# Performance work log

Hardware: AMD Instinct MI355X
Metric: run time of the kernel (lower is better)

Reference implementation:

```python
import jax, jax.numpy as jnp
import numpy as np
from jax import lax

D_MODEL = 1024
D_FF = 4096
NUM_EXPERTS = 24
TOP_K = 2
B, S = 2, 2048


def setup_inputs() -> dict:
    key = jax.random.key(0)
    ks = jax.random.split(key, 5)
    x = jax.random.normal(ks[0], (B, S, D_MODEL), dtype=jnp.float32)
    gate_w = jax.random.normal(ks[1], (D_MODEL, NUM_EXPERTS), dtype=jnp.float32) * 0.02
    gate_b = jnp.zeros((NUM_EXPERTS,), dtype=jnp.float32)
    w1 = jax.random.normal(ks[2], (NUM_EXPERTS, D_MODEL, D_FF), dtype=jnp.float32) * 0.02
    b1 = jnp.zeros((NUM_EXPERTS, D_FF), dtype=jnp.float32)
    w2 = jax.random.normal(ks[3], (NUM_EXPERTS, D_FF, D_MODEL), dtype=jnp.float32) * 0.02
    b2 = jnp.zeros((NUM_EXPERTS, D_MODEL), dtype=jnp.float32)
    return {"x": x, "gate_w": gate_w, "gate_b": gate_b,
            "w1": w1, "b1": b1, "w2": w2, "b2": b2}


def reference(x, gate_w, gate_b, w1, b1, w2, b2):
    b, s, d = x.shape
    t = b * s
    xf = x.reshape(t, d)  # [T, d]
    scores = xf @ gate_w + gate_b  # [T, E]
    top_val, top_idx = lax.top_k(scores, TOP_K)  # [T, k]
    prob = jax.nn.softmax(top_val, axis=-1)  # softmax over the top-k logits
    # scatter top-k probabilities into dense per-expert combine weights [T, E]
    combine = jnp.zeros((t, NUM_EXPERTS), dtype=x.dtype)
    combine = combine.at[jnp.arange(t)[:, None], top_idx].add(prob)

    def body(acc, expert):
        w1e, b1e, w2e, b2e, ce = expert  # ce: [T]
        h = jax.nn.gelu(xf @ w1e + b1e, approximate=False)  # exact GELU as torch default
        y = h @ w2e + b2e  # [T, d]
        return acc + ce[:, None] * y, None

    out, _ = lax.scan(body, jnp.zeros_like(xf), (w1, b1, w2, b2, combine.T))
    return out.reshape(b, s, d)
```

## Files before the change

### kernel.cpp

```cpp
#include <hip/hip_runtime.h>
#include <math.h>

#define DM 1024
#define DF 4096
#define NE 24
#define T_TOK 4096
#define T2 (T_TOK*2)

#define BM 128
#define BN 128
#define BK 64
#define MTILES 8
#define NK1 (DM / BK)
#define NK2 (DF / BK)

typedef __attribute__((ext_vector_type(4))) float f32x4;
typedef __attribute__((ext_vector_type(2))) float f32x2;
typedef __attribute__((ext_vector_type(8))) short s16x8;

static __device__ __forceinline__ unsigned short f2bf(float f) {
    unsigned int u = __float_as_uint(f);
    unsigned int r = u + 0x7fffu + ((u >> 16) & 1u);
    return (unsigned short)(r >> 16);
}

static __device__ __forceinline__ unsigned int cvtpk(float lo, float hi) {
    unsigned int r;
    asm("v_cvt_pk_bf16_f32 %0, %1, %2" : "=v"(r) : "v"(lo), "v"(hi));
    return r;
}

#define GLL(gsrc, ldst)                                                          \
    __builtin_amdgcn_global_load_lds(                                            \
        (const __attribute__((address_space(1))) void*)(gsrc),                   \
        (__attribute__((address_space(3))) void*)(ldst), 16, 0, 0)


__global__ void k_transpose_gw(const float* __restrict__ gw, float* __restrict__ gwT) {
    int e = blockIdx.x;
    for (int d = threadIdx.x; d < DM; d += blockDim.x)
        gwT[e * DM + d] = gw[d * NE + e];
}

__global__ void k_gate(const float* __restrict__ x, const float* __restrict__ gwT,
                       const float* __restrict__ gb,
                       int* __restrict__ idx, float* __restrict__ prob) {
    int wave = threadIdx.x >> 6;
    int lane = threadIdx.x & 63;
    int t = blockIdx.x * 4 + wave;
    if (t >= T_TOK) return;
    const float* xr = x + (size_t)t * DM;
    float acc[NE];
#pragma unroll
    for (int e = 0; e < NE; e++) acc[e] = 0.f;
    for (int i = 0; i < DM / 64; i++) {
        int d = lane + i * 64;
        float xv = xr[d];
#pragma unroll
        for (int e = 0; e < NE; e++) acc[e] = fmaf(xv, gwT[e * DM + d], acc[e]);
    }
#pragma unroll
    for (int e = 0; e < NE; e++) {
        float v = acc[e];
        for (int off = 32; off >= 1; off >>= 1) v += __shfl_xor(v, off);
        acc[e] = v;
    }
    if (lane == 0) {
        float v1 = -1e30f, v2 = -1e30f;
        int i1 = -1, i2 = -1;
        for (int e = 0; e < NE; e++) {
            float s = acc[e] + gb[e];
            if (s > v1) { v2 = v1; i2 = i1; v1 = s; i1 = e; }
            else if (s > v2) { v2 = s; i2 = e; }
        }
        float e2 = expf(v2 - v1);
        float inv = 1.f / (1.f + e2);
        idx[t * 2] = i1; idx[t * 2 + 1] = i2;
        prob[t * 2] = inv; prob[t * 2 + 1] = e2 * inv;
    }
}


__global__ __launch_bounds__(1024)
void k_route(const int* __restrict__ idx, int* __restrict__ counts,
             int* __restrict__ offsets, int* __restrict__ slot_tok,
             int* __restrict__ pair_slot) {
    __shared__ int cnt[NE], offs[NE], cur[NE];
    const int tid = threadIdx.x;
    if (tid < NE) cnt[tid] = 0;
    __syncthreads();
    for (int i = tid; i < T2; i += 1024) atomicAdd(&cnt[idx[i]], 1);
    __syncthreads();
    if (tid == 0) {
        int s = 0;
        for (int e = 0; e < NE; e++) {
            offs[e] = s; offsets[e] = s; counts[e] = cnt[e]; s += cnt[e];
        }
    }
    if (tid < NE) cur[tid] = 0;
    __syncthreads();
    for (int i = tid; i < T2; i += 1024) {
        int e = idx[i];
        int pos = offs[e] + atomicAdd(&cur[e], 1);
        slot_tok[pos] = i >> 1;
        pair_slot[i] = pos;
    }
}

__global__ void k_gather(const float* __restrict__ x, const int* __restrict__ slot_tok,
                         unsigned short* __restrict__ Xg) {
    int s = blockIdx.x;
    int tok = slot_tok[s];
    const float4* src = (const float4*)(x + (size_t)tok * DM);
    ushort4* dst = (ushort4*)(Xg + (size_t)s * DM);
    for (int i = threadIdx.x; i < DM / 4; i += blockDim.x) {
        float4 v = src[i];
        ushort4 o;
        o.x = f2bf(v.x); o.y = f2bf(v.y); o.z = f2bf(v.z); o.w = f2bf(v.w);
        dst[i] = o;
    }
}

__global__ void k_combine(const float* __restrict__ Y, const int* __restrict__ pair_slot,
                          const float* __restrict__ prob, const int* __restrict__ idx,
                          const float* __restrict__ b2, float* __restrict__ out) {
    int t = blockIdx.x;
    int s1 = pair_slot[t * 2], s2 = pair_slot[t * 2 + 1];
    int e1 = idx[t * 2], e2 = idx[t * 2 + 1];
    float p1 = prob[t * 2], p2 = prob[t * 2 + 1];
    const float4* y1 = (const float4*)(Y + (size_t)s1 * DM);
    const float4* y2 = (const float4*)(Y + (size_t)s2 * DM);
    const float4* ba = (const float4*)(b2 + (size_t)e1 * DM);
    const float4* bb = (const float4*)(b2 + (size_t)e2 * DM);
    float4* o = (float4*)(out + (size_t)t * DM);
    int i = threadIdx.x;
    float4 a = y1[i], b = y2[i], c = ba[i], d = bb[i];
    float4 r;
    r.x = p1 * (a.x + c.x) + p2 * (b.x + d.x);
    r.y = p1 * (a.y + c.y) + p2 * (b.y + d.y);
    r.z = p1 * (a.z + c.z) + p2 * (b.z + d.z);
    r.w = p1 * (a.w + c.w) + p2 * (b.w + d.w);
    o[i] = r;
}


__global__ __launch_bounds__(512)
void k_mm1(const unsigned short* __restrict__ Xg, const float* __restrict__ w1,
           const float* __restrict__ b1, const int* __restrict__ counts,
           const int* __restrict__ offsets, unsigned short* __restrict__ H) {
    const int TOT = NE * MTILES * (DF / BN);
    int work = (blockIdx.x & 7) * (TOT >> 3) + (blockIdx.x >> 3);
    const int mt = work % MTILES;
    const int en = work / MTILES;
    const int e  = en >> 5;
    const int n0 = (en & 31) * BN;
    const int ne = counts[e];
    const int m0 = mt * BM;
    if (m0 >= ne) return;
    const int rows = min(BM, ne - m0);
    const int slotbase = offsets[e] + m0;

    __shared__ unsigned short As[2][BM * BK];
    __shared__ unsigned short Bs[BN * BK];

    const int tid  = threadIdx.x;
    const int lane = tid & 63;
    const int w    = tid >> 6;
    const int wm   = w >> 1, wn = w & 1;

    const float* w1e = w1 + (size_t)e * DM * DF;
    const int arow = lane >> 3;
    const int gchunk = ((lane & 7) ^ arow) * 8;

    const int swz0 = ((lane >> 4) ^ (lane & 7)) << 4;
    const int swz1 = ((4 | (lane >> 4)) ^ (lane & 7)) << 4;
    const char* Arow0 = (const char*)As[0] + (wm * 32 + (lane & 15)) * 128;
    const char* Arow1 = (const char*)As[1] + (wm * 32 + (lane & 15)) * 128;
    const char* Brow  = (const char*)Bs + (wn * 64 + (lane & 15)) * 128;

    const int np = (tid & 63) * 2;
    const int ckw = w;
    char* BsW0 = (char*)Bs + (np + 0) * 128 + ((ckw ^ ((np + 0) & 7)) << 4);
    char* BsW1 = (char*)Bs + (np + 1) * 128 + ((ckw ^ ((np + 1) & 7)) << 4);

    f32x4 acc[2][4];
#pragma unroll
    for (int a = 0; a < 2; a++)
#pragma unroll
        for (int b = 0; b < 4; b++) acc[a][b] = (f32x4)0.f;

    f32x2 L[8];
    auto loadB = [&](int k0) {
#pragma unroll
        for (int j = 0; j < 8; j++)
            L[j] = *(const f32x2*)(w1e + (size_t)(k0 + w * 8 + j) * DF + n0 + np);
    };
    auto stageA = [&](int buf, int k0) {
#pragma unroll
        for (int q = 0; q < 2; q++) {
            int row = (w * 2 + q) * 8 + arow;
            GLL(Xg + (size_t)(slotbase + row) * DM + k0 + gchunk,
                &As[buf][(w * 2 + q) * 512]);
        }
    };

    stageA(0, 0);
    loadB(0);
#pragma unroll 1
    for (int kt = 0; kt < NK1; ++kt) {
        const int cur = kt & 1;
        __syncthreads();
        if (kt + 1 < NK1) stageA(cur ^ 1, (kt + 1) * BK);
        {
            uint4 v0, v1;
            v0.x = cvtpk(L[0][0], L[1][0]);
            v0.y = cvtpk(L[2][0], L[3][0]);
            v0.z = cvtpk(L[4][0], L[5][0]);
            v0.w = cvtpk(L[6][0], L[7][0]);
            v1.x = cvtpk(L[0][1], L[1][1]);
            v1.y = cvtpk(L[2][1], L[3][1]);
            v1.z = cvtpk(L[4][1], L[5][1]);
            v1.w = cvtpk(L[6][1], L[7][1]);
            *(uint4*)BsW0 = v0;
            *(uint4*)BsW1 = v1;
        }
        if (kt + 1 < NK1) loadB((kt + 1) * BK);
        const char* Arow = cur ? Arow1 : Arow0;
        s16x8 af[2][2];
#pragma unroll
        for (int f = 0; f < 2; f++) {
            af[0][f] = *(const s16x8*)(Arow + f * 2048 + swz0);
            af[1][f] = *(const s16x8*)(Arow + f * 2048 + swz1);
        }
        asm volatile("s_waitcnt lgkmcnt(0)" ::: "memory");
        __builtin_amdgcn_s_barrier();
        __builtin_amdgcn_sched_barrier(0);
        s16x8 bfr[2][4];
#pragma unroll
        for (int f = 0; f < 4; f++) {
            bfr[0][f] = *(const s16x8*)(Brow + f * 2048 + swz0);
            bfr[1][f] = *(const s16x8*)(Brow + f * 2048 + swz1);
        }
#pragma unroll
        for (int ks = 0; ks < 2; ks++)
#pragma unroll
            for (int fm = 0; fm < 2; fm++)
#pragma unroll
                for (int fn = 0; fn < 4; fn++)
                    acc[fm][fn] = __builtin_amdgcn_mfma_f32_16x16x32_bf16(
                        af[ks][fm], bfr[ks][fn], acc[fm][fn], 0, 0, 0);
    }

    const float* b1e = b1 + (size_t)e * DF;
#pragma unroll
    for (int fm = 0; fm < 2; fm++) {
        const int mrow = wm * 32 + fm * 16 + ((lane >> 4) << 2);
#pragma unroll
        for (int fn = 0; fn < 4; fn++) {
            const int ncol = n0 + wn * 64 + fn * 16 + (lane & 15);
            const float bb = b1e[ncol];
#pragma unroll
            for (int r = 0; r < 4; r++) {
                const int m = mrow + r;
                if (m < rows) {
                    float h = acc[fm][fn][r] + bb;
                    h = 0.5f * h * (1.f + erff(h * 0.70710678118654752f));
                    H[(size_t)(slotbase + m) * DF + ncol] = f2bf(h);
                }
            }
        }
    }
}

__global__ __launch_bounds__(512)
void k_mm2(const unsigned short* __restrict__ Hb, const float* __restrict__ w2,
           const int* __restrict__ counts, const int* __restrict__ offsets,
           float* __restrict__ Y) {
    const int TOT = NE * MTILES * (DM / BN);
    int work = (blockIdx.x & 7) * (TOT >> 3) + (blockIdx.x >> 3);
    const int mt = work % MTILES;
    const int en = work / MTILES;
    const int e  = en >> 3;
    const int n0 = (en & 7) * BN;
    const int ne = counts[e];
    const int m0 = mt * BM;
    if (m0 >= ne) return;
    const int rows = min(BM, ne - m0);
    const int slotbase = offsets[e] + m0;

    __shared__ unsigned short As[2][BM * BK];
    __shared__ unsigned short Bs[BN * BK];

    const int tid  = threadIdx.x;
    const int lane = tid & 63;
    const int w    = tid >> 6;
    const int wm   = w >> 1, wn = w & 1;

    const float* w2e = w2 + (size_t)e * DF * DM;
    const int arow = lane >> 3;
    const int gchunk = ((lane & 7) ^ arow) * 8;

    const int swz0 = ((lane >> 4) ^ (lane & 7)) << 4;
    const int swz1 = ((4 | (lane >> 4)) ^ (lane & 7)) << 4;
    const char* Arow0 = (const char*)As[0] + (wm * 32 + (lane & 15)) * 128;
    const char* Arow1 = (const char*)As[1] + (wm * 32 + (lane & 15)) * 128;
    const char* Brow  = (const char*)Bs + (wn * 64 + (lane & 15)) * 128;

    const int np = (tid & 63) * 2;
    const int ckw = w;
    char* BsW0 = (char*)Bs + (np + 0) * 128 + ((ckw ^ ((np + 0) & 7)) << 4);
    char* BsW1 = (char*)Bs + (np + 1) * 128 + ((ckw ^ ((np + 1) & 7)) << 4);

    f32x4 acc[2][4];
#pragma unroll
    for (int a = 0; a < 2; a++)
#pragma unroll
        for (int b = 0; b < 4; b++) acc[a][b] = (f32x4)0.f;

    f32x2 L[8];
    auto loadB = [&](int k0) {
#pragma unroll
        for (int j = 0; j < 8; j++)
            L[j] = *(const f32x2*)(w2e + (size_t)(k0 + w * 8 + j) * DM + n0 + np);
    };
    auto stageA = [&](int buf, int k0) {
#pragma unroll
        for (int q = 0; q < 2; q++) {
            int row = (w * 2 + q) * 8 + arow;
            GLL(Hb + (size_t)(slotbase + row) * DF + k0 + gchunk,
                &As[buf][(w * 2 + q) * 512]);
        }
    };

    stageA(0, 0);
    loadB(0);
#pragma unroll 1
    for (int kt = 0; kt < NK2; ++kt) {
        const int cur = kt & 1;
        __syncthreads();
        if (kt + 1 < NK2) stageA(cur ^ 1, (kt + 1) * BK);
        {
            uint4 v0, v1;
            v0.x = cvtpk(L[0][0], L[1][0]);
            v0.y = cvtpk(L[2][0], L[3][0]);
            v0.z = cvtpk(L[4][0], L[5][0]);
            v0.w = cvtpk(L[6][0], L[7][0]);
            v1.x = cvtpk(L[0][1], L[1][1]);
            v1.y = cvtpk(L[2][1], L[3][1]);
            v1.z = cvtpk(L[4][1], L[5][1]);
            v1.w = cvtpk(L[6][1], L[7][1]);
            *(uint4*)BsW0 = v0;
            *(uint4*)BsW1 = v1;
        }
        if (kt + 1 < NK2) loadB((kt + 1) * BK);
        const char* Arow = cur ? Arow1 : Arow0;
        s16x8 af[2][2];
#pragma unroll
        for (int f = 0; f < 2; f++) {
            af[0][f] = *(const s16x8*)(Arow + f * 2048 + swz0);
            af[1][f] = *(const s16x8*)(Arow + f * 2048 + swz1);
        }
        asm volatile("s_waitcnt lgkmcnt(0)" ::: "memory");
        __builtin_amdgcn_s_barrier();
        __builtin_amdgcn_sched_barrier(0);
        s16x8 bfr[2][4];
#pragma unroll
        for (int f = 0; f < 4; f++) {
            bfr[0][f] = *(const s16x8*)(Brow + f * 2048 + swz0);
            bfr[1][f] = *(const s16x8*)(Brow + f * 2048 + swz1);
        }
#pragma unroll
        for (int ks = 0; ks < 2; ks++)
#pragma unroll
            for (int fm = 0; fm < 2; fm++)
#pragma unroll
                for (int fn = 0; fn < 4; fn++)
                    acc[fm][fn] = __builtin_amdgcn_mfma_f32_16x16x32_bf16(
                        af[ks][fm], bfr[ks][fn], acc[fm][fn], 0, 0, 0);
    }

#pragma unroll
    for (int fm = 0; fm < 2; fm++) {
        const int mrow = wm * 32 + fm * 16 + ((lane >> 4) << 2);
#pragma unroll
        for (int fn = 0; fn < 4; fn++) {
            const int ncol = n0 + wn * 64 + fn * 16 + (lane & 15);
#pragma unroll
            for (int r = 0; r < 4; r++) {
                const int m = mrow + r;
                if (m < rows)
                    Y[(size_t)(slotbase + m) * DM + ncol] = acc[fm][fn][r];
            }
        }
    }
}


extern "C" void kernel_launch(void* const* d_in, const int* in_sizes, int n_in,
                              void* d_out, int out_size, void* d_ws, size_t ws_size,
                              hipStream_t stream) {
    const float* x   = (const float*)d_in[0];
    const float* gw  = (const float*)d_in[1];
    const float* gb  = (const float*)d_in[2];
    const float* w1  = (const float*)d_in[3];
    const float* b1  = (const float*)d_in[4];
    const float* w2  = (const float*)d_in[5];
    const float* b2  = (const float*)d_in[6];
    float* out = (float*)d_out;

    size_t off = 0;
    auto alloc = [&](size_t bytes) {
        void* p = (char*)d_ws + off;
        off += (bytes + 255) & ~(size_t)255;
        return p;
    };
    float* gwT       = (float*)alloc(NE * DM * sizeof(float));
    int*   idx       = (int*)alloc(T2 * sizeof(int));
    float* prob      = (float*)alloc(T2 * sizeof(float));
    int*   counts    = (int*)alloc(32 * sizeof(int));
    int*   offsets   = (int*)alloc(32 * sizeof(int));
    int*   slot_tok  = (int*)alloc(T2 * sizeof(int));
    int*   pair_slot = (int*)alloc(T2 * sizeof(int));
    unsigned short* Xg = (unsigned short*)alloc((size_t)(T2 + BM) * DM * sizeof(unsigned short));
    unsigned short* Hb = (unsigned short*)alloc((size_t)(T2 + BM) * DF * sizeof(unsigned short));
    float* Yb        = (float*)alloc((size_t)(T2 + BM) * DM * sizeof(float));

    k_transpose_gw<<<NE, 256, 0, stream>>>(gw, gwT);
    k_gate<<<T_TOK / 4, 256, 0, stream>>>(x, gwT, gb, idx, prob);
    k_route<<<1, 1024, 0, stream>>>(idx, counts, offsets, slot_tok, pair_slot);
    k_gather<<<T2, 256, 0, stream>>>(x, slot_tok, Xg);

    k_mm1<<<NE * MTILES * (DF / BN), 512, 0, stream>>>(Xg, w1, b1, counts, offsets, Hb);
    k_mm2<<<NE * MTILES * (DM / BN), 512, 0, stream>>>(Hb, w2, counts, offsets, Yb);
    k_combine<<<T_TOK, 256, 0, stream>>>(Yb, pair_slot, prob, idx, b2, out);
}
```

Before: 533.3 us.

## Use 4-wave blocks with larger per-wave tiles and split-K the second GEMM

Both expert GEMMs drop from 512 to 256 threads per block, so each wave computes a 64x64 output sub-tile and loads twice as much A and B per k-step. The second GEMM is split into two halves along its K dimension, writing two partial output buffers that the combine kernel sums. This doubles the number of blocks for mm2 to fill the machine better and shortens each block's K loop. The cost is an extra fp32 partial buffer to write and read, plus higher register pressure from the 4x4 accumulator tiles.

```diff
diff --git a/kernel.cpp b/kernel.cpp
--- a/kernel.cpp
+++ b/kernel.cpp
@@ -12,7 +12,7 @@
 #define BK 64
 #define MTILES 8
 #define NK1 (DM / BK)
-#define NK2 (DF / BK)
+#define NK2H (DF / BK / 2)
 
 typedef __attribute__((ext_vector_type(4))) float f32x4;
 typedef __attribute__((ext_vector_type(2))) float f32x2;
@@ -121,30 +121,34 @@
     }
 }
 
-__global__ void k_combine(const float* __restrict__ Y, const int* __restrict__ pair_slot,
+__global__ void k_combine(const float* __restrict__ Y1, const float* __restrict__ Y2,
+                          const int* __restrict__ pair_slot,
                           const float* __restrict__ prob, const int* __restrict__ idx,
                           const float* __restrict__ b2, float* __restrict__ out) {
     int t = blockIdx.x;
     int s1 = pair_slot[t * 2], s2 = pair_slot[t * 2 + 1];
     int e1 = idx[t * 2], e2 = idx[t * 2 + 1];
     float p1 = prob[t * 2], p2 = prob[t * 2 + 1];
-    const float4* y1 = (const float4*)(Y + (size_t)s1 * DM);
-    const float4* y2 = (const float4*)(Y + (size_t)s2 * DM);
+    const float4* y1a = (const float4*)(Y1 + (size_t)s1 * DM);
+    const float4* y1b = (const float4*)(Y2 + (size_t)s1 * DM);
+    const float4* y2a = (const float4*)(Y1 + (size_t)s2 * DM);
+    const float4* y2b = (const float4*)(Y2 + (size_t)s2 * DM);
     const float4* ba = (const float4*)(b2 + (size_t)e1 * DM);
     const float4* bb = (const float4*)(b2 + (size_t)e2 * DM);
     float4* o = (float4*)(out + (size_t)t * DM);
     int i = threadIdx.x;
-    float4 a = y1[i], b = y2[i], c = ba[i], d = bb[i];
+    float4 a0 = y1a[i], a1 = y1b[i], b0 = y2a[i], b1 = y2b[i];
+    float4 c = ba[i], d = bb[i];
     float4 r;
-    r.x = p1 * (a.x + c.x) + p2 * (b.x + d.x);
-    r.y = p1 * (a.y + c.y) + p2 * (b.y + d.y);
-    r.z = p1 * (a.z + c.z) + p2 * (b.z + d.z);
-    r.w = p1 * (a.w + c.w) + p2 * (b.w + d.w);
+    r.x = p1 * (a0.x + a1.x + c.x) + p2 * (b0.x + b1.x + d.x);
+    r.y = p1 * (a0.y + a1.y + c.y) + p2 * (b0.y + b1.y + d.y);
+    r.z = p1 * (a0.z + a1.z + c.z) + p2 * (b0.z + b1.z + d.z);
+    r.w = p1 * (a0.w + a1.w + c.w) + p2 * (b0.w + b1.w + d.w);
     o[i] = r;
 }
 
 
-__global__ __launch_bounds__(512)
+__global__ __launch_bounds__(256)
 void k_mm1(const unsigned short* __restrict__ Xg, const float* __restrict__ w1,
            const float* __restrict__ b1, const int* __restrict__ counts,
            const int* __restrict__ offsets, unsigned short* __restrict__ H) {
@@ -174,33 +178,34 @@
 
     const int swz0 = ((lane >> 4) ^ (lane & 7)) << 4;
     const int swz1 = ((4 | (lane >> 4)) ^ (lane & 7)) << 4;
-    const char* Arow0 = (const char*)As[0] + (wm * 32 + (lane & 15)) * 128;
-    const char* Arow1 = (const char*)As[1] + (wm * 32 + (lane & 15)) * 128;
+    const char* Arow0 = (const char*)As[0] + (wm * 64 + (lane & 15)) * 128;
+    const char* Arow1 = (const char*)As[1] + (wm * 64 + (lane & 15)) * 128;
     const char* Brow  = (const char*)Bs + (wn * 64 + (lane & 15)) * 128;
 
     const int np = (tid & 63) * 2;
-    const int ckw = w;
-    char* BsW0 = (char*)Bs + (np + 0) * 128 + ((ckw ^ ((np + 0) & 7)) << 4);
-    char* BsW1 = (char*)Bs + (np + 1) * 128 + ((ckw ^ ((np + 1) & 7)) << 4);
-
-    f32x4 acc[2][4];
-#pragma unroll
-    for (int a = 0; a < 2; a++)
+    char* BsW0a = (char*)Bs + (np + 0) * 128 + (((w * 2 + 0) ^ ((np + 0) & 7)) << 4);
+    char* BsW0b = (char*)Bs + (np + 0) * 128 + (((w * 2 + 1) ^ ((np + 0) & 7)) << 4);
+    char* BsW1a = (char*)Bs + (np + 1) * 128 + (((w * 2 + 0) ^ ((np + 1) & 7)) << 4);
+    char* BsW1b = (char*)Bs + (np + 1) * 128 + (((w * 2 + 1) ^ ((np + 1) & 7)) << 4);
+
+    f32x4 acc[4][4];
+#pragma unroll
+    for (int a = 0; a < 4; a++)
 #pragma unroll
         for (int b = 0; b < 4; b++) acc[a][b] = (f32x4)0.f;
 
-    f32x2 L[8];
+    f32x2 L[16];
     auto loadB = [&](int k0) {
 #pragma unroll
-        for (int j = 0; j < 8; j++)
-            L[j] = *(const f32x2*)(w1e + (size_t)(k0 + w * 8 + j) * DF + n0 + np);
+        for (int j = 0; j < 16; j++)
+            L[j] = *(const f32x2*)(w1e + (size_t)(k0 + w * 16 + j) * DF + n0 + np);
     };
     auto stageA = [&](int buf, int k0) {
 #pragma unroll
-        for (int q = 0; q < 2; q++) {
-            int row = (w * 2 + q) * 8 + arow;
+        for (int q = 0; q < 4; q++) {
+            int row = (w * 4 + q) * 8 + arow;
             GLL(Xg + (size_t)(slotbase + row) * DM + k0 + gchunk,
-                &As[buf][(w * 2 + q) * 512]);
+                &As[buf][(w * 4 + q) * 512]);
         }
     };
 
@@ -212,23 +217,25 @@
         __syncthreads();
         if (kt + 1 < NK1) stageA(cur ^ 1, (kt + 1) * BK);
         {
-            uint4 v0, v1;
-            v0.x = cvtpk(L[0][0], L[1][0]);
-            v0.y = cvtpk(L[2][0], L[3][0]);
-            v0.z = cvtpk(L[4][0], L[5][0]);
-            v0.w = cvtpk(L[6][0], L[7][0]);
-            v1.x = cvtpk(L[0][1], L[1][1]);
-            v1.y = cvtpk(L[2][1], L[3][1]);
-            v1.z = cvtpk(L[4][1], L[5][1]);
-            v1.w = cvtpk(L[6][1], L[7][1]);
-            *(uint4*)BsW0 = v0;
-            *(uint4*)BsW1 = v1;
+            uint4 v;
+            v.x = cvtpk(L[0][0], L[1][0]);  v.y = cvtpk(L[2][0], L[3][0]);
+            v.z = cvtpk(L[4][0], L[5][0]);  v.w = cvtpk(L[6][0], L[7][0]);
+            *(uint4*)BsW0a = v;
+            v.x = cvtpk(L[8][0], L[9][0]);  v.y = cvtpk(L[10][0], L[11][0]);
+            v.z = cvtpk(L[12][0], L[13][0]); v.w = cvtpk(L[14][0], L[15][0]);
+            *(uint4*)BsW0b = v;
+            v.x = cvtpk(L[0][1], L[1][1]);  v.y = cvtpk(L[2][1], L[3][1]);
+            v.z = cvtpk(L[4][1], L[5][1]);  v.w = cvtpk(L[6][1], L[7][1]);
+            *(uint4*)BsW1a = v;
+            v.x = cvtpk(L[8][1], L[9][1]);  v.y = cvtpk(L[10][1], L[11][1]);
+            v.z = cvtpk(L[12][1], L[13][1]); v.w = cvtpk(L[14][1], L[15][1]);
+            *(uint4*)BsW1b = v;
         }
         if (kt + 1 < NK1) loadB((kt + 1) * BK);
         const char* Arow = cur ? Arow1 : Arow0;
-        s16x8 af[2][2];
-#pragma unroll
-        for (int f = 0; f < 2; f++) {
+        s16x8 af[2][4];
+#pragma unroll
+        for (int f = 0; f < 4; f++) {
             af[0][f] = *(const s16x8*)(Arow + f * 2048 + swz0);
             af[1][f] = *(const s16x8*)(Arow + f * 2048 + swz1);
         }
@@ -244,7 +251,7 @@
 #pragma unroll
         for (int ks = 0; ks < 2; ks++)
 #pragma unroll
-            for (int fm = 0; fm < 2; fm++)
+            for (int fm = 0; fm < 4; fm++)
 #pragma unroll
                 for (int fn = 0; fn < 4; fn++)
                     acc[fm][fn] = __builtin_amdgcn_mfma_f32_16x16x32_bf16(
@@ -253,8 +260,8 @@
 
     const float* b1e = b1 + (size_t)e * DF;
 #pragma unroll
-    for (int fm = 0; fm < 2; fm++) {
-        const int mrow = wm * 32 + fm * 16 + ((lane >> 4) << 2);
+    for (int fm = 0; fm < 4; fm++) {
+        const int mrow = wm * 64 + fm * 16 + ((lane >> 4) << 2);
 #pragma unroll
         for (int fn = 0; fn < 4; fn++) {
             const int ncol = n0 + wn * 64 + fn * 16 + (lane & 15);
@@ -272,14 +279,16 @@
     }
 }
 
-__global__ __launch_bounds__(512)
+__global__ __launch_bounds__(256)
 void k_mm2(const unsigned short* __restrict__ Hb, const float* __restrict__ w2,
            const int* __restrict__ counts, const int* __restrict__ offsets,
-           float* __restrict__ Y) {
-    const int TOT = NE * MTILES * (DM / BN);
+           float* __restrict__ Y1, float* __restrict__ Y2) {
+    const int TOT = NE * MTILES * (DM / BN) * 2;
     int work = (blockIdx.x & 7) * (TOT >> 3) + (blockIdx.x >> 3);
     const int mt = work % MTILES;
-    const int en = work / MTILES;
+    int rest = work / MTILES;
+    const int ksl = rest & 1;
+    const int en = rest >> 1;
     const int e  = en >> 3;
     const int n0 = (en & 7) * BN;
     const int ne = counts[e];
@@ -287,6 +296,8 @@
     if (m0 >= ne) return;
     const int rows = min(BM, ne - m0);
     const int slotbase = offsets[e] + m0;
+    const int kbeg = ksl * (DF / 2);
+    float* Y = ksl ? Y2 : Y1;
 
     __shared__ unsigned short As[2][BM * BK];
     __shared__ unsigned short Bs[BN * BK];
@@ -302,61 +313,64 @@
 
     const int swz0 = ((lane >> 4) ^ (lane & 7)) << 4;
     const int swz1 = ((4 | (lane >> 4)) ^ (lane & 7)) << 4;
-    const char* Arow0 = (const char*)As[0] + (wm * 32 + (lane & 15)) * 128;
-    const char* Arow1 = (const char*)As[1] + (wm * 32 + (lane & 15)) * 128;
+    const char* Arow0 = (const char*)As[0] + (wm * 64 + (lane & 15)) * 128;
+    const char* Arow1 = (const char*)As[1] + (wm * 64 + (lane & 15)) * 128;
     const char* Brow  = (const char*)Bs + (wn * 64 + (lane & 15)) * 128;
 
     const int np = (tid & 63) * 2;
-    const int ckw = w;
-    char* BsW0 = (char*)Bs + (np + 0) * 128 + ((ckw ^ ((np + 0) & 7)) << 4);
-    char* BsW1 = (char*)Bs + (np + 1) * 128 + ((ckw ^ ((np + 1) & 7)) << 4);
-
-    f32x4 acc[2][4];
-#pragma unroll
-    for (int a = 0; a < 2; a++)
+    char* BsW0a = (char*)Bs + (np + 0) * 128 + (((w * 2 + 0) ^ ((np + 0) & 7)) << 4);
+    char* BsW0b = (char*)Bs + (np + 0) * 128 + (((w * 2 + 1) ^ ((np + 0) & 7)) << 4);
+    char* BsW1a = (char*)Bs + (np + 1) * 128 + (((w * 2 + 0) ^ ((np + 1) & 7)) << 4);
+    char* BsW1b = (char*)Bs + (np + 1) * 128 + (((w * 2 + 1) ^ ((np + 1) & 7)) << 4);
+
+    f32x4 acc[4][4];
+#pragma unroll
+    for (int a = 0; a < 4; a++)
 #pragma unroll
         for (int b = 0; b < 4; b++) acc[a][b] = (f32x4)0.f;
 
-    f32x2 L[8];
+    f32x2 L[16];
     auto loadB = [&](int k0) {
 #pragma unroll
-        for (int j = 0; j < 8; j++)
-            L[j] = *(const f32x2*)(w2e + (size_t)(k0 + w * 8 + j) * DM + n0 + np);
+        for (int j = 0; j < 16; j++)
+            L[j] = *(const f32x2*)(w2e + (size_t)(k0 + w * 16 + j) * DM + n0 + np);
     };
     auto stageA = [&](int buf, int k0) {
 #pragma unroll
-        for (int q = 0; q < 2; q++) {
-            int row = (w * 2 + q) * 8 + arow;
+        for (int q = 0; q < 4; q++) {
+            int row = (w * 4 + q) * 8 + arow;
             GLL(Hb + (size_t)(slotbase + row) * DF + k0 + gchunk,
-                &As[buf][(w * 2 + q) * 512]);
+                &As[buf][(w * 4 + q) * 512]);
         }
     };
 
-    stageA(0, 0);
-    loadB(0);
+    stageA(0, kbeg);
+    loadB(kbeg);
 #pragma unroll 1
-    for (int kt = 0; kt < NK2; ++kt) {
+    for (int kt = 0; kt < NK2H; ++kt) {
         const int cur = kt & 1;
         __syncthreads();
-        if (kt + 1 < NK2) stageA(cur ^ 1, (kt + 1) * BK);
+        if (kt + 1 < NK2H) stageA(cur ^ 1, kbeg + (kt + 1) * BK);
         {
-            uint4 v0, v1;
-            v0.x = cvtpk(L[0][0], L[1][0]);
-            v0.y = cvtpk(L[2][0], L[3][0]);
-            v0.z = cvtpk(L[4][0], L[5][0]);
-            v0.w = cvtpk(L[6][0], L[7][0]);
-            v1.x = cvtpk(L[0][1], L[1][1]);
-            v1.y = cvtpk(L[2][1], L[3][1]);
-            v1.z = cvtpk(L[4][1], L[5][1]);
-            v1.w = cvtpk(L[6][1], L[7][1]);
-            *(uint4*)BsW0 = v0;
-            *(uint4*)BsW1 = v1;
-        }
-        if (kt + 1 < NK2) loadB((kt + 1) * BK);
+            uint4 v;
+            v.x = cvtpk(L[0][0], L[1][0]);  v.y = cvtpk(L[2][0], L[3][0]);
+            v.z = cvtpk(L[4][0], L[5][0]);  v.w = cvtpk(L[6][0], L[7][0]);
+            *(uint4*)BsW0a = v;
+            v.x = cvtpk(L[8][0], L[9][0]);  v.y = cvtpk(L[10][0], L[11][0]);
+            v.z = cvtpk(L[12][0], L[13][0]); v.w = cvtpk(L[14][0], L[15][0]);
+            *(uint4*)BsW0b = v;
+            v.x = cvtpk(L[0][1], L[1][1]);  v.y = cvtpk(L[2][1], L[3][1]);
+            v.z = cvtpk(L[4][1], L[5][1]);  v.w = cvtpk(L[6][1], L[7][1]);
+            *(uint4*)BsW1a = v;
+            v.x = cvtpk(L[8][1], L[9][1]);  v.y = cvtpk(L[10][1], L[11][1]);
+            v.z = cvtpk(L[12][1], L[13][1]); v.w = cvtpk(L[14][1], L[15][1]);
+            *(uint4*)BsW1b = v;
+        }
+        if (kt + 1 < NK2H) loadB(kbeg + (kt + 1) * BK);
         const char* Arow = cur ? Arow1 : Arow0;
-        s16x8 af[2][2];
-#pragma unroll
-        for (int f = 0; f < 2; f++) {
+        s16x8 af[2][4];
+#pragma unroll
+        for (int f = 0; f < 4; f++) {
             af[0][f] = *(const s16x8*)(Arow + f * 2048 + swz0);
             af[1][f] = *(const s16x8*)(Arow + f * 2048 + swz1);
         }
@@ -372,7 +386,7 @@
 #pragma unroll
         for (int ks = 0; ks < 2; ks++)
 #pragma unroll
-            for (int fm = 0; fm < 2; fm++)
+            for (int fm = 0; fm < 4; fm++)
 #pragma unroll
                 for (int fn = 0; fn < 4; fn++)
                     acc[fm][fn] = __builtin_amdgcn_mfma_f32_16x16x32_bf16(
@@ -380,8 +394,8 @@
     }
 
 #pragma unroll
-    for (int fm = 0; fm < 2; fm++) {
-        const int mrow = wm * 32 + fm * 16 + ((lane >> 4) << 2);
+    for (int fm = 0; fm < 4; fm++) {
+        const int mrow = wm * 64 + fm * 16 + ((lane >> 4) << 2);
 #pragma unroll
         for (int fn = 0; fn < 4; fn++) {
             const int ncol = n0 + wn * 64 + fn * 16 + (lane & 15);
@@ -424,13 +438,14 @@
     unsigned short* Xg = (unsigned short*)alloc((size_t)(T2 + BM) * DM * sizeof(unsigned short));
     unsigned short* Hb = (unsigned short*)alloc((size_t)(T2 + BM) * DF * sizeof(unsigned short));
     float* Yb        = (float*)alloc((size_t)(T2 + BM) * DM * sizeof(float));
+    float* Yb2       = (float*)alloc((size_t)(T2 + BM) * DM * sizeof(float));
 
     k_transpose_gw<<<NE, 256, 0, stream>>>(gw, gwT);
     k_gate<<<T_TOK / 4, 256, 0, stream>>>(x, gwT, gb, idx, prob);
     k_route<<<1, 1024, 0, stream>>>(idx, counts, offsets, slot_tok, pair_slot);
     k_gather<<<T2, 256, 0, stream>>>(x, slot_tok, Xg);
 
-    k_mm1<<<NE * MTILES * (DF / BN), 512, 0, stream>>>(Xg, w1, b1, counts, offsets, Hb);
-    k_mm2<<<NE * MTILES * (DM / BN), 512, 0, stream>>>(Hb, w2, counts, offsets, Yb);
-    k_combine<<<T_TOK, 256, 0, stream>>>(Yb, pair_slot, prob, idx, b2, out);
-}
+    k_mm1<<<NE * MTILES * (DF / BN), 256, 0, stream>>>(Xg, w1, b1, counts, offsets, Hb);
+    k_mm2<<<NE * MTILES * (DM / BN) * 2, 256, 0, stream>>>(Hb, w2, counts, offsets, Yb, Yb2);
+    k_combine<<<T_TOK, 256, 0, stream>>>(Yb, Yb2, pair_slot, prob, idx, b2, out);
+}
```

Result: slower. 549.9 us (+3.1%).

## Split mm2 reduction dimension in two and sum partials in combine

Applied to the files above, without the earlier changes.

The second expert GEMM is split along its K dimension (DF) into two halves, each written to a separate fp32 partial buffer, which doubles the number of workgroups. The combine kernel now reads both partials per slot and adds them before applying the bias and routing weights. The aim is more parallelism and better CU occupancy for mm2, since many tiles are empty or partial under uneven expert load. In exchange it adds an extra fp32 output buffer, more writes from mm2 and more reads in combine.

```diff
diff --git a/kernel.cpp b/kernel.cpp
--- a/kernel.cpp
+++ b/kernel.cpp
@@ -12,7 +12,7 @@
 #define BK 64
 #define MTILES 8
 #define NK1 (DM / BK)
-#define NK2 (DF / BK)
+#define NK2H (DF / BK / 2)
 
 typedef __attribute__((ext_vector_type(4))) float f32x4;
 typedef __attribute__((ext_vector_type(2))) float f32x2;
@@ -121,25 +121,29 @@
     }
 }
 
-__global__ void k_combine(const float* __restrict__ Y, const int* __restrict__ pair_slot,
+__global__ void k_combine(const float* __restrict__ Y1, const float* __restrict__ Y2,
+                          const int* __restrict__ pair_slot,
                           const float* __restrict__ prob, const int* __restrict__ idx,
                           const float* __restrict__ b2, float* __restrict__ out) {
     int t = blockIdx.x;
     int s1 = pair_slot[t * 2], s2 = pair_slot[t * 2 + 1];
     int e1 = idx[t * 2], e2 = idx[t * 2 + 1];
     float p1 = prob[t * 2], p2 = prob[t * 2 + 1];
-    const float4* y1 = (const float4*)(Y + (size_t)s1 * DM);
-    const float4* y2 = (const float4*)(Y + (size_t)s2 * DM);
+    const float4* y1a = (const float4*)(Y1 + (size_t)s1 * DM);
+    const float4* y1b = (const float4*)(Y2 + (size_t)s1 * DM);
+    const float4* y2a = (const float4*)(Y1 + (size_t)s2 * DM);
+    const float4* y2b = (const float4*)(Y2 + (size_t)s2 * DM);
     const float4* ba = (const float4*)(b2 + (size_t)e1 * DM);
     const float4* bb = (const float4*)(b2 + (size_t)e2 * DM);
     float4* o = (float4*)(out + (size_t)t * DM);
     int i = threadIdx.x;
-    float4 a = y1[i], b = y2[i], c = ba[i], d = bb[i];
+    float4 a0 = y1a[i], a1 = y1b[i], b0 = y2a[i], b1 = y2b[i];
+    float4 c = ba[i], d = bb[i];
     float4 r;
-    r.x = p1 * (a.x + c.x) + p2 * (b.x + d.x);
-    r.y = p1 * (a.y + c.y) + p2 * (b.y + d.y);
-    r.z = p1 * (a.z + c.z) + p2 * (b.z + d.z);
-    r.w = p1 * (a.w + c.w) + p2 * (b.w + d.w);
+    r.x = p1 * (a0.x + a1.x + c.x) + p2 * (b0.x + b1.x + d.x);
+    r.y = p1 * (a0.y + a1.y + c.y) + p2 * (b0.y + b1.y + d.y);
+    r.z = p1 * (a0.z + a1.z + c.z) + p2 * (b0.z + b1.z + d.z);
+    r.w = p1 * (a0.w + a1.w + c.w) + p2 * (b0.w + b1.w + d.w);
     o[i] = r;
 }
 
@@ -275,11 +279,13 @@
 __global__ __launch_bounds__(512)
 void k_mm2(const unsigned short* __restrict__ Hb, const float* __restrict__ w2,
            const int* __restrict__ counts, const int* __restrict__ offsets,
-           float* __restrict__ Y) {
-    const int TOT = NE * MTILES * (DM / BN);
+           float* __restrict__ Y1, float* __restrict__ Y2) {
+    const int TOT = NE * MTILES * (DM / BN) * 2;
     int work = (blockIdx.x & 7) * (TOT >> 3) + (blockIdx.x >> 3);
     const int mt = work % MTILES;
-    const int en = work / MTILES;
+    int rest = work / MTILES;
+    const int ksl = rest & 1;
+    const int en = rest >> 1;
     const int e  = en >> 3;
     const int n0 = (en & 7) * BN;
     const int ne = counts[e];
@@ -287,6 +293,8 @@
     if (m0 >= ne) return;
     const int rows = min(BM, ne - m0);
     const int slotbase = offsets[e] + m0;
+    const int kbeg = ksl * (DF / 2);
+    float* Y = ksl ? Y2 : Y1;
 
     __shared__ unsigned short As[2][BM * BK];
     __shared__ unsigned short Bs[BN * BK];
@@ -332,13 +340,13 @@
         }
     };
 
-    stageA(0, 0);
-    loadB(0);
+    stageA(0, kbeg);
+    loadB(kbeg);
 #pragma unroll 1
-    for (int kt = 0; kt < NK2; ++kt) {
+    for (int kt = 0; kt < NK2H; ++kt) {
         const int cur = kt & 1;
         __syncthreads();
-        if (kt + 1 < NK2) stageA(cur ^ 1, (kt + 1) * BK);
+        if (kt + 1 < NK2H) stageA(cur ^ 1, kbeg + (kt + 1) * BK);
         {
             uint4 v0, v1;
             v0.x = cvtpk(L[0][0], L[1][0]);
@@ -352,7 +360,7 @@
             *(uint4*)BsW0 = v0;
             *(uint4*)BsW1 = v1;
         }
-        if (kt + 1 < NK2) loadB((kt + 1) * BK);
+        if (kt + 1 < NK2H) loadB(kbeg + (kt + 1) * BK);
         const char* Arow = cur ? Arow1 : Arow0;
         s16x8 af[2][2];
 #pragma unroll
@@ -424,6 +432,7 @@
     unsigned short* Xg = (unsigned short*)alloc((size_t)(T2 + BM) * DM * sizeof(unsigned short));
     unsigned short* Hb = (unsigned short*)alloc((size_t)(T2 + BM) * DF * sizeof(unsigned short));
     float* Yb        = (float*)alloc((size_t)(T2 + BM) * DM * sizeof(float));
+    float* Yb2       = (float*)alloc((size_t)(T2 + BM) * DM * sizeof(float));
 
     k_transpose_gw<<<NE, 256, 0, stream>>>(gw, gwT);
     k_gate<<<T_TOK / 4, 256, 0, stream>>>(x, gwT, gb, idx, prob);
@@ -431,6 +440,6 @@
     k_gather<<<T2, 256, 0, stream>>>(x, slot_tok, Xg);
 
     k_mm1<<<NE * MTILES * (DF / BN), 512, 0, stream>>>(Xg, w1, b1, counts, offsets, Hb);
-    k_mm2<<<NE * MTILES * (DM / BN), 512, 0, stream>>>(Hb, w2, counts, offsets, Yb);
-    k_combine<<<T_TOK, 256, 0, stream>>>(Yb, pair_slot, prob, idx, b2, out);
-}
+    k_mm2<<<NE * MTILES * (DM / BN) * 2, 512, 0, stream>>>(Hb, w2, counts, offsets, Yb, Yb2);
+    k_combine<<<T_TOK, 256, 0, stream>>>(Yb, Yb2, pair_slot, prob, idx, b2, out);
+}
```

New measurement: 519.2 us. 1.03x faster.
